# Kernel tuning notes

Hardware: AMD Instinct MI355X
Metric: run time of the kernel (lower is better)

## Reference

```python
import jax, jax.numpy as jnp
import numpy as np

RADIUS = 0.3      # extents/2, extents = radius_scale*6*particle_radius = 4*6*0.025 = 0.6
KSIZE = 4         # kernel_size [4,4,4]
KMAX = 80         # padded neighbor count
N = 50000
BOX = 5.2         # box side -> ~40 neighbors within RADIUS on average
CIN = 3
COUT = 3
_PI = 3.14159265358979323846


def _build_neighbors(pos, radius, kmax):
    # fixed-radius search (L2), ignore_query_point=True, padded to kmax per row
    n = pos.shape[0]
    r2 = radius * radius
    sq = (pos * pos).sum(1)
    idx = np.zeros((n, kmax), np.int32)
    msk = np.zeros((n, kmax), np.bool_)
    ch = 2500
    for s in range(0, n, ch):
        e = min(s + ch, n)
        d2 = sq[s:e, None] + sq[None, :] - 2.0 * (pos[s:e] @ pos.T)
        d2[np.arange(e - s), np.arange(s, e)] = np.inf  # radius_search_ignore_query_points
        rows, cols = np.nonzero(d2 < r2)
        starts = np.searchsorted(rows, np.arange(e - s))
        slot = np.arange(len(rows)) - starts[rows]
        keep = slot < kmax
        idx[rows[keep] + s, slot[keep]] = cols[keep]
        msk[rows[keep] + s, slot[keep]] = True
    return idx, msk


def setup_inputs():
    key = jax.random.key(0)
    k1, k2, k3 = jax.random.split(key, 3)
    pos = jax.random.uniform(k1, (N, 3), jnp.float32) * BOX
    vel = jax.random.normal(k2, (N, 3), jnp.float32)
    # keras 'uniform' initializer: U(-0.05, 0.05)
    kernel = jax.random.uniform(k3, (KSIZE, KSIZE, KSIZE, CIN, COUT), jnp.float32, -0.05, 0.05)
    nidx, nmask = _build_neighbors(np.asarray(pos), RADIUS, KMAX)
    return {"pos": pos, "vel": vel, "kernel": kernel,
            "neighbor_idx": jnp.asarray(nidx), "neighbor_mask": jnp.asarray(nmask)}


def _ball_to_cube_volume_preserving(u):
    # Open3D CoordinateTransformation.h: MapSphereToCylinder then MapCylinderToCube
    eps = 1e-12
    x, y, z = u[..., 0], u[..., 1], u[..., 2]
    sq = x * x + y * y + z * z
    norm = jnp.sqrt(jnp.maximum(sq, eps))
    sq_xy = x * x + y * y
    # sphere -> cylinder
    top = (1.25 * z * z) > sq_xy
    s_top = jnp.sqrt(3.0 * norm / (norm + jnp.abs(z)))
    s_side = norm / jnp.sqrt(jnp.maximum(sq_xy, eps))
    x1 = jnp.where(top, x * s_top, x * s_side)
    y1 = jnp.where(top, y * s_top, y * s_side)
    z1 = jnp.where(top, jnp.sign(z) * norm, 1.5 * z)
    small = sq < eps
    x1 = jnp.where(small, x, x1)
    y1 = jnp.where(small, y, y1)
    z1 = jnp.where(small, z, z1)
    # cylinder -> cube (equal-area disc->square on xy)
    sq_xy1 = x1 * x1 + y1 * y1
    norm_xy = jnp.sqrt(jnp.maximum(sq_xy1, eps))
    xbig = jnp.abs(y1) <= jnp.abs(x1)
    sx = jnp.sign(x1) * norm_xy
    sy = jnp.sign(y1) * norm_xy
    safe_x = jnp.where(jnp.abs(x1) > eps, x1, 1.0)
    safe_y = jnp.where(jnp.abs(y1) > eps, y1, 1.0)
    x2 = jnp.where(xbig, sx, sy * (4.0 / _PI) * jnp.arctan(x1 / safe_y))
    y2 = jnp.where(xbig, sx * (4.0 / _PI) * jnp.arctan(y1 / safe_x), sy)
    small_xy = sq_xy1 < eps
    x2 = jnp.where(small_xy, x1, x2)
    y2 = jnp.where(small_xy, y1, y2)
    return x2, y2, z1


def _grid_coords(c):
    # align_corners=True: [-1,1] -> [0, KSIZE-1]; 'linear' interpolation clamps to border
    t = jnp.clip((c + 1.0) * (0.5 * (KSIZE - 1)), 0.0, KSIZE - 1.0)
    t0 = jnp.floor(t)
    i0 = t0.astype(jnp.int32)
    i1 = jnp.minimum(i0 + 1, KSIZE - 1)
    f = t - t0
    return (i0, i1), (1.0 - f, f)


def _cconv(pos, vel, kernel, neighbor_idx, neighbor_mask):
    n = pos.shape[0]
    rel = pos[neighbor_idx] - pos[:, None, :]              # [N,K,3]
    d2 = jnp.sum(rel * rel, -1)
    # window_poly6 on squared distance normalized by radius^2
    imp = jnp.clip((1.0 - d2 / (RADIUS * RADIUS)) ** 3, 0.0, 1.0)
    imp = imp * neighbor_mask.astype(vel.dtype)
    cx, cy, cz = _ball_to_cube_volume_preserving(rel / RADIUS)
    (xi0, xi1), (wx0, wx1) = _grid_coords(cx)
    (yi0, yi1), (wy0, wy1) = _grid_coords(cy)
    (zi0, zi1), (wz0, wz1) = _grid_coords(cz)
    phi = vel[neighbor_idx] * imp[..., None]               # [N,K,Cin]
    rows = jnp.arange(n)[:, None]
    # accumulate window*trilinear-weighted features into the 64 filter taps,
    # then contract once with the flattened kernel (math identical to per-pair
    # interp(W) @ feat since everything is linear)
    A = jnp.zeros((n, KSIZE * KSIZE * KSIZE, vel.shape[1]), vel.dtype)
    for zi, wz in ((zi0, wz0), (zi1, wz1)):
        for yi, wy in ((yi0, wy0), (yi1, wy1)):
            for xi, wx in ((xi0, wx0), (xi1, wx1)):
                corner = (zi * KSIZE + yi) * KSIZE + xi
                A = A.at[rows, corner].add((wz * wy * wx)[..., None] * phi)
    Wflat = kernel.reshape(KSIZE * KSIZE * KSIZE, kernel.shape[3], kernel.shape[4])
    return jnp.einsum('ngi,gio->no', A, Wflat)        # [N, COUT]


def reference(pos, vel, kernel, neighbor_idx, neighbor_mask):
    return _cconv(pos, vel, kernel, neighbor_idx, neighbor_mask)
```

## Files before the change

### kernel.cpp

```cpp
#include <hip/hip_runtime.h>
#include <math.h>

#define N_PART 50000
#define KMAX 80
#define KS 4
#define LPP 16
#define MAXTRIP 5

typedef __attribute__((ext_vector_type(8))) _Float16 h8;
typedef __attribute__((ext_vector_type(2))) _Float16 h2;

__global__ __launch_bounds__(256) void pack_pv_kernel(
    const float* __restrict__ pos, const float* __restrict__ vel,
    float4* __restrict__ pv4)
{
    int p = blockIdx.x * blockDim.x + threadIdx.x;
    if (p >= N_PART) return;
    float4 a = make_float4(pos[3*p], pos[3*p+1], pos[3*p+2], vel[3*p]);
    float4 b = make_float4(vel[3*p+1], vel[3*p+2], 0.0f, 0.0f);
    pv4[2*p]     = a;
    pv4[2*p + 1] = b;
}

template <typename MT>
__device__ __forceinline__ int prefix_count(const MT* __restrict__ nmask, int base, int sub) {
    int lc = 0; bool more = true;
    #pragma unroll
    for (int i = 0; i < 5; ++i) {
        bool t = nmask[base + sub * 5 + i] != 0;
        lc += (more && t) ? 1 : 0;
        more = more && t;
    }
    bool full = (lc == 5);
    unsigned long long nb = __ballot(!full);
    int wl  = threadIdx.x & 63;
    int grp = wl >> 4;
    unsigned int gb = (unsigned int)((nb >> (16 * grp)) & 0xFFFFull);
    if (gb == 0) return KMAX;
    int fi  = __ffs(gb) - 1;
    int flc = __shfl(lc, (grp << 4) + fi, 64);
    return fi * 5 + flc;
}

__device__ __forceinline__ float atan_poly(float t) {
    float t2 = t * t;
    float p = -0.01172120f;
    p = p * t2 + 0.05265332f;
    p = p * t2 - 0.11643287f;
    p = p * t2 + 0.19354346f;
    p = p * t2 - 0.33262347f;
    p = p * t2 + 0.99997726f;
    return t * p;
}

template <bool PACKED>
__global__ __launch_bounds__(256) void cconv_kernel(
    const float* __restrict__ pos,
    const float* __restrict__ vel,
    const float4* __restrict__ pv4,
    const float* __restrict__ Wg,
    const int* __restrict__ nidx,
    const void* __restrict__ nmask,
    float* __restrict__ out)
{
    __shared__ _Float16 WsH[64 * 8];
    __shared__ float    Ws8[64];
    for (int t = threadIdx.x; t < 64 * 8; t += blockDim.x) {
        int g = t >> 3, r = t & 7;
        WsH[t] = (_Float16)Wg[g * 9 + r];
    }
    for (int t = threadIdx.x; t < 64; t += blockDim.x)
        Ws8[t] = Wg[t * 9 + 8];
    __syncthreads();

    int gid = blockIdx.x * blockDim.x + threadIdx.x;
    int p   = gid / LPP;
    int sub = gid & (LPP - 1);
    if (p >= N_PART) return;

    const int base = p * KMAX;

    int idxs[MAXTRIP];
    #pragma unroll
    for (int j = 0; j < MAXTRIP; ++j)
        idxs[j] = nidx[base + sub + j * LPP];

    bool byteMask;
    {
        const unsigned* mw = (const unsigned*)nmask;
        int lane = threadIdx.x & 63;
        bool big = false;
        #pragma unroll
        for (int i = 0; i < 8; ++i)
            big |= (mw[lane + 64 * i] > 1u);
        byteMask = (__ballot(big) != 0ULL);
    }

    float4 a, b;
    float  cpx, cpy, cpz;
    if (PACKED) {
        a = pv4[2 * idxs[0]];
        b = pv4[2 * idxs[0] + 1];
        float4 c = pv4[2 * p];
        cpx = c.x; cpy = c.y; cpz = c.z;
    } else {
        int i0 = idxs[0];
        a = make_float4(pos[i0*3], pos[i0*3+1], pos[i0*3+2], vel[i0*3]);
        b = make_float4(vel[i0*3+1], vel[i0*3+2], 0.f, 0.f);
        cpx = pos[p * 3 + 0]; cpy = pos[p * 3 + 1]; cpz = pos[p * 3 + 2];
    }

    int cnt;
    if (byteMask) cnt = prefix_count<unsigned char>((const unsigned char*)nmask, base, sub);
    else          cnt = prefix_count<int>((const int*)nmask, base, sub);

    int trips = (cnt > sub) ? ((cnt - sub + LPP - 1) >> 4) : 0;

    const float inv_r = 1.0f / 0.3f;
    const float eps   = 1e-12f;
    const float FOUR_OVER_PI = 1.27323954473516268615f;

    float acc0 = 0.0f, acc1 = 0.0f, acc2 = 0.0f;

    for (int j = 0; j < trips; ++j) {
        int jn = (j + 1 < MAXTRIP) ? j + 1 : MAXTRIP - 1;
        float4 an, bn;
        if (PACKED) {
            an = pv4[2 * idxs[jn]];
            bn = pv4[2 * idxs[jn] + 1];
        } else {
            int ii = idxs[jn];
            an = make_float4(pos[ii*3], pos[ii*3+1], pos[ii*3+2], vel[ii*3]);
            bn = make_float4(vel[ii*3+1], vel[ii*3+2], 0.f, 0.f);
        }

        float rx = (a.x - cpx) * inv_r;
        float ry = (a.y - cpy) * inv_r;
        float rz = (a.z - cpz) * inv_r;
        float ux = a.w, uy = b.x, uz = b.y;

        float sq = rx * rx + ry * ry + rz * rz;

        float t1  = 1.0f - sq;
        float imp = fminf(fmaxf(t1 * t1 * t1, 0.0f), 1.0f);

        float norm  = sqrtf(fmaxf(sq, eps));
        float sq_xy = rx * rx + ry * ry;
        bool  top   = (1.25f * rz * rz) > sq_xy;
        float s_top  = sqrtf(3.0f * norm * __builtin_amdgcn_rcpf(norm + fabsf(rz)));
        float s_side = norm * __builtin_amdgcn_rsqf(fmaxf(sq_xy, eps));
        float s  = top ? s_top : s_side;
        float x1 = rx * s;
        float y1 = ry * s;
        float z1 = top ? copysignf(norm, rz) : 1.5f * rz;
        if (sq < eps) { x1 = rx; y1 = ry; z1 = rz; }

        float sq_xy1  = x1 * x1 + y1 * y1;
        float norm_xy = sqrtf(fmaxf(sq_xy1, eps));
        bool  xbig = fabsf(y1) <= fabsf(x1);
        float num  = xbig ? y1 : x1;
        float den  = xbig ? x1 : y1;
        float sden = (fabsf(den) > eps) ? den : 1.0f;
        float t    = num * __builtin_amdgcn_rcpf(sden);
        float at   = atan_poly(t);
        float sd   = copysignf(norm_xy, den);
        float u    = sd * FOUR_OVER_PI * at;
        float x2   = xbig ? sd : u;
        float y2   = xbig ? u  : sd;
        if (sq_xy1 < eps) { x2 = x1; y2 = y1; }

        float tx = fminf(fmaxf((x2 + 1.0f) * 1.5f, 0.0f), 3.0f);
        float ty = fminf(fmaxf((y2 + 1.0f) * 1.5f, 0.0f), 3.0f);
        float tz = fminf(fmaxf((z1 + 1.0f) * 1.5f, 0.0f), 3.0f);
        float fx0 = floorf(tx), fy0 = floorf(ty), fz0 = floorf(tz);
        int xi0 = (int)fx0, yi0 = (int)fy0, zi0 = (int)fz0;
        int xi1 = min(xi0 + 1, KS - 1);
        int yi1 = min(yi0 + 1, KS - 1);
        int zi1 = min(zi0 + 1, KS - 1);
        float wx1 = tx - fx0, wx0 = 1.0f - wx1;
        float wy1 = ty - fy0, wy0 = 1.0f - wy1;
        float wz1 = tz - fz0, wz0 = 1.0f - wz1;

        int   zi[2] = { zi0, zi1 };  float wzv[2] = { wz0, wz1 };
        int   yi[2] = { yi0, yi1 };  float wyv[2] = { wy0, wy1 };
        int   xi[2] = { xi0, xi1 };  float wxv[2] = { wx0, wx1 };

        h2 M01 = (h2)(_Float16)0.0f;
        h2 M23 = (h2)(_Float16)0.0f;
        h2 M45 = (h2)(_Float16)0.0f;
        h2 M67 = (h2)(_Float16)0.0f;
        float m8 = 0.0f;

        #pragma unroll
        for (int cz = 0; cz < 2; ++cz) {
            #pragma unroll
            for (int cy = 0; cy < 2; ++cy) {
                float wzy = wzv[cz] * wyv[cy];
                #pragma unroll
                for (int cx = 0; cx < 2; ++cx) {
                    int corner = (zi[cz] * KS + yi[cy]) * KS + xi[cx];
                    h8 wv = *(const h8*)&WsH[corner << 3];
                    float wf = wzy * wxv[cx];
                    _Float16 wh = (_Float16)wf;
                    h2 ww = { wh, wh };
                    M01 += ww * __builtin_shufflevector(wv, wv, 0, 1);
                    M23 += ww * __builtin_shufflevector(wv, wv, 2, 3);
                    M45 += ww * __builtin_shufflevector(wv, wv, 4, 5);
                    M67 += ww * __builtin_shufflevector(wv, wv, 6, 7);
                    m8  += wf * Ws8[corner];
                }
            }
        }

        float m0 = (float)M01[0], m1 = (float)M01[1];
        float m2 = (float)M23[0], m3 = (float)M23[1];
        float m4 = (float)M45[0], m5 = (float)M45[1];
        float m6 = (float)M67[0], m7 = (float)M67[1];
        float s0 = ux * m0 + uy * m3 + uz * m6;
        float s1 = ux * m1 + uy * m4 + uz * m7;
        float s2 = ux * m2 + uy * m5 + uz * m8;
        acc0 += imp * s0;
        acc1 += imp * s1;
        acc2 += imp * s2;

        a = an; b = bn;
    }

    acc0 += __shfl_xor(acc0, 1); acc0 += __shfl_xor(acc0, 2);
    acc0 += __shfl_xor(acc0, 4); acc0 += __shfl_xor(acc0, 8);
    acc1 += __shfl_xor(acc1, 1); acc1 += __shfl_xor(acc1, 2);
    acc1 += __shfl_xor(acc1, 4); acc1 += __shfl_xor(acc1, 8);
    acc2 += __shfl_xor(acc2, 1); acc2 += __shfl_xor(acc2, 2);
    acc2 += __shfl_xor(acc2, 4); acc2 += __shfl_xor(acc2, 8);

    if (sub == 0) {
        out[p * 3 + 0] = acc0;
        out[p * 3 + 1] = acc1;
        out[p * 3 + 2] = acc2;
    }
}

extern "C" void kernel_launch(void* const* d_in, const int* in_sizes, int n_in,
                              void* d_out, int out_size, void* d_ws, size_t ws_size,
                              hipStream_t stream) {
    const float* pos   = (const float*)d_in[0];
    const float* vel   = (const float*)d_in[1];
    const float* Wg    = (const float*)d_in[2];
    const int*   nidx  = (const int*)d_in[3];
    const void*  nmask = d_in[4];
    float*       out   = (float*)d_out;

    size_t pv_off = 256;
    size_t need   = pv_off + (size_t)N_PART * 8 * sizeof(float);
    bool   packed = ws_size >= need;
    float4* pv4   = (float4*)((char*)d_ws + pv_off);

    if (packed) {
        pack_pv_kernel<<<(N_PART + 255) / 256, 256, 0, stream>>>(pos, vel, pv4);
    }

    int threads = 256;
    long long total = (long long)N_PART * LPP;
    int grid = (int)((total + threads - 1) / threads);
    if (packed) {
        cconv_kernel<true><<<grid, threads, 0, stream>>>(pos, vel, pv4, Wg, nidx, nmask, out);
    } else {
        cconv_kernel<false><<<grid, threads, 0, stream>>>(pos, vel, (const float4*)nullptr, Wg, nidx, nmask, out);
    }
}
```

Measured before the change: 33.77 us.

## Drop pack kernel and process two neighbors per iteration with deeper prefetch

Removes the separate pos/vel packing kernel and its launch, reading the pos and vel arrays directly with scalar loads instead. The neighbor loop is unrolled by two and prefetches two neighbors' data ahead, masking the second pair's contribution when it falls past the valid count. This aims to cut a kernel launch and an extra global pass, and to raise memory-level parallelism per thread. The costs are unaligned scalar gathers replacing float4 loads, more registers, and wasted work on masked pairs.

```diff
diff --git a/kernel.cpp b/kernel.cpp
--- a/kernel.cpp
+++ b/kernel.cpp
@@ -5,21 +5,19 @@
 #define KMAX 80
 #define KS 4
 #define LPP 16
-#define MAXTRIP 5
 
 typedef __attribute__((ext_vector_type(8))) _Float16 h8;
 typedef __attribute__((ext_vector_type(2))) _Float16 h2;
 
-__global__ __launch_bounds__(256) void pack_pv_kernel(
-    const float* __restrict__ pos, const float* __restrict__ vel,
-    float4* __restrict__ pv4)
-{
-    int p = blockIdx.x * blockDim.x + threadIdx.x;
-    if (p >= N_PART) return;
-    float4 a = make_float4(pos[3*p], pos[3*p+1], pos[3*p+2], vel[3*p]);
-    float4 b = make_float4(vel[3*p+1], vel[3*p+2], 0.0f, 0.0f);
-    pv4[2*p]     = a;
-    pv4[2*p + 1] = b;
+__device__ __forceinline__ float atan_poly(float t) {
+    float t2 = t * t;
+    float p = -0.01172120f;
+    p = p * t2 + 0.05265332f;
+    p = p * t2 - 0.11643287f;
+    p = p * t2 + 0.19354346f;
+    p = p * t2 - 0.33262347f;
+    p = p * t2 + 0.99997726f;
+    return t * p;
 }
 
 template <typename MT>
@@ -42,22 +40,116 @@
     return fi * 5 + flc;
 }
 
-__device__ __forceinline__ float atan_poly(float t) {
-    float t2 = t * t;
-    float p = -0.01172120f;
-    p = p * t2 + 0.05265332f;
-    p = p * t2 - 0.11643287f;
-    p = p * t2 + 0.19354346f;
-    p = p * t2 - 0.33262347f;
-    p = p * t2 + 0.99997726f;
-    return t * p;
-}
-
-template <bool PACKED>
+struct PV { float px, py, pz, ux, uy, uz; };
+
+__device__ __forceinline__ void load_pv(const float* __restrict__ pos,
+                                        const float* __restrict__ vel,
+                                        int i, PV& v) {
+    v.px = pos[3*i];  v.py = pos[3*i+1];  v.pz = pos[3*i+2];
+    v.ux = vel[3*i];  v.uy = vel[3*i+1];  v.uz = vel[3*i+2];
+}
+
+__device__ __forceinline__ void pair_contrib(
+    const PV& n, float cpx, float cpy, float cpz, float vmask,
+    const _Float16* __restrict__ WsH, const float* __restrict__ Ws8,
+    float& acc0, float& acc1, float& acc2)
+{
+    const float inv_r = 1.0f / 0.3f;
+    const float eps   = 1e-12f;
+    const float FOUR_OVER_PI = 1.27323954473516268615f;
+
+    float rx = (n.px - cpx) * inv_r;
+    float ry = (n.py - cpy) * inv_r;
+    float rz = (n.pz - cpz) * inv_r;
+
+    float sq = rx * rx + ry * ry + rz * rz;
+
+    float t1  = 1.0f - sq;
+    float imp = fminf(fmaxf(t1 * t1 * t1, 0.0f), 1.0f) * vmask;
+
+    float norm  = sqrtf(fmaxf(sq, eps));
+    float sq_xy = rx * rx + ry * ry;
+    bool  top   = (1.25f * rz * rz) > sq_xy;
+    float s_top  = sqrtf(3.0f * norm * __builtin_amdgcn_rcpf(norm + fabsf(rz)));
+    float s_side = norm * __builtin_amdgcn_rsqf(fmaxf(sq_xy, eps));
+    float s  = top ? s_top : s_side;
+    float x1 = rx * s;
+    float y1 = ry * s;
+    float z1 = top ? copysignf(norm, rz) : 1.5f * rz;
+    if (sq < eps) { x1 = rx; y1 = ry; z1 = rz; }
+
+    float sq1 = x1 * x1 + y1 * y1;
+    float nxy = sqrtf(fmaxf(sq1, eps));
+    bool  xb  = fabsf(y1) <= fabsf(x1);
+    float num = xb ? y1 : x1;
+    float den = xb ? x1 : y1;
+    float sden = (fabsf(den) > eps) ? den : 1.0f;
+    float t    = num * __builtin_amdgcn_rcpf(sden);
+    float at   = atan_poly(t);
+    float sd   = copysignf(nxy, den);
+    float u    = sd * FOUR_OVER_PI * at;
+    float x2   = xb ? sd : u;
+    float y2   = xb ? u  : sd;
+    if (sq1 < eps) { x2 = x1; y2 = y1; }
+
+    float tx = fminf(fmaxf((x2 + 1.0f) * 1.5f, 0.0f), 3.0f);
+    float ty = fminf(fmaxf((y2 + 1.0f) * 1.5f, 0.0f), 3.0f);
+    float tz = fminf(fmaxf((z1 + 1.0f) * 1.5f, 0.0f), 3.0f);
+    float fx0 = floorf(tx), fy0 = floorf(ty), fz0 = floorf(tz);
+    int xi0 = (int)fx0, yi0 = (int)fy0, zi0 = (int)fz0;
+    int xi1 = min(xi0 + 1, KS - 1);
+    int yi1 = min(yi0 + 1, KS - 1);
+    int zi1 = min(zi0 + 1, KS - 1);
+    float wx1 = tx - fx0, wx0 = 1.0f - wx1;
+    float wy1 = ty - fy0, wy0 = 1.0f - wy1;
+    float wz1 = tz - fz0, wz0 = 1.0f - wz1;
+
+    int   zia[2] = { zi0, zi1 };  float wza[2] = { wz0, wz1 };
+    int   yia[2] = { yi0, yi1 };  float wya[2] = { wy0, wy1 };
+    int   xia[2] = { xi0, xi1 };  float wxa[2] = { wx0, wx1 };
+
+    h2 M01 = (h2)(_Float16)0.0f;
+    h2 M23 = (h2)(_Float16)0.0f;
+    h2 M45 = (h2)(_Float16)0.0f;
+    h2 M67 = (h2)(_Float16)0.0f;
+    float m8 = 0.0f;
+
+    #pragma unroll
+    for (int cz = 0; cz < 2; ++cz) {
+        #pragma unroll
+        for (int cy = 0; cy < 2; ++cy) {
+            float wzy = wza[cz] * wya[cy];
+            #pragma unroll
+            for (int cx = 0; cx < 2; ++cx) {
+                int corner = (zia[cz] * KS + yia[cy]) * KS + xia[cx];
+                h8 wv = *(const h8*)&WsH[corner << 3];
+                float wf = wzy * wxa[cx];
+                _Float16 wh = (_Float16)wf;
+                h2 ww = { wh, wh };
+                M01 += ww * __builtin_shufflevector(wv, wv, 0, 1);
+                M23 += ww * __builtin_shufflevector(wv, wv, 2, 3);
+                M45 += ww * __builtin_shufflevector(wv, wv, 4, 5);
+                M67 += ww * __builtin_shufflevector(wv, wv, 6, 7);
+                m8  += wf * Ws8[corner];
+            }
+        }
+    }
+
+    float m0 = (float)M01[0], m1 = (float)M01[1];
+    float m2 = (float)M23[0], m3 = (float)M23[1];
+    float m4 = (float)M45[0], m5 = (float)M45[1];
+    float m6 = (float)M67[0], m7 = (float)M67[1];
+    float s0 = n.ux * m0 + n.uy * m3 + n.uz * m6;
+    float s1 = n.ux * m1 + n.uy * m4 + n.uz * m7;
+    float s2 = n.ux * m2 + n.uy * m5 + n.uz * m8;
+    acc0 += imp * s0;
+    acc1 += imp * s1;
+    acc2 += imp * s2;
+}
+
 __global__ __launch_bounds__(256) void cconv_kernel(
     const float* __restrict__ pos,
     const float* __restrict__ vel,
-    const float4* __restrict__ pv4,
     const float* __restrict__ Wg,
     const int* __restrict__ nidx,
     const void* __restrict__ nmask,
@@ -74,16 +166,16 @@
     __syncthreads();
 
     int gid = blockIdx.x * blockDim.x + threadIdx.x;
-    int p   = gid / LPP;
-    int sub = gid & (LPP - 1);
+    int p   = gid >> 4;
+    int sub = gid & 15;
     if (p >= N_PART) return;
 
     const int base = p * KMAX;
 
-    int idxs[MAXTRIP];
+    int idxs[5];
     #pragma unroll
-    for (int j = 0; j < MAXTRIP; ++j)
-        idxs[j] = nidx[base + sub + j * LPP];
+    for (int m = 0; m < 5; ++m)
+        idxs[m] = nidx[base + sub + (m << 4)];
 
     bool byteMask;
     {
@@ -96,134 +188,34 @@
         byteMask = (__ballot(big) != 0ULL);
     }
 
-    float4 a, b;
-    float  cpx, cpy, cpz;
-    if (PACKED) {
-        a = pv4[2 * idxs[0]];
-        b = pv4[2 * idxs[0] + 1];
-        float4 c = pv4[2 * p];
-        cpx = c.x; cpy = c.y; cpz = c.z;
-    } else {
-        int i0 = idxs[0];
-        a = make_float4(pos[i0*3], pos[i0*3+1], pos[i0*3+2], vel[i0*3]);
-        b = make_float4(vel[i0*3+1], vel[i0*3+2], 0.f, 0.f);
-        cpx = pos[p * 3 + 0]; cpy = pos[p * 3 + 1]; cpz = pos[p * 3 + 2];
-    }
+    float cpx = pos[3 * p], cpy = pos[3 * p + 1], cpz = pos[3 * p + 2];
 
     int cnt;
     if (byteMask) cnt = prefix_count<unsigned char>((const unsigned char*)nmask, base, sub);
     else          cnt = prefix_count<int>((const int*)nmask, base, sub);
 
-    int trips = (cnt > sub) ? ((cnt - sub + LPP - 1) >> 4) : 0;
-
-    const float inv_r = 1.0f / 0.3f;
-    const float eps   = 1e-12f;
-    const float FOUR_OVER_PI = 1.27323954473516268615f;
+    int rem   = cnt - sub;
+    int trips = (rem > 0) ? ((rem + 31) >> 5) : 0;
+
+    PV A0, A1, A0n, A1n;
+    load_pv(pos, vel, idxs[0], A0);
+    load_pv(pos, vel, idxs[1], A1);
 
     float acc0 = 0.0f, acc1 = 0.0f, acc2 = 0.0f;
 
     for (int j = 0; j < trips; ++j) {
-        int jn = (j + 1 < MAXTRIP) ? j + 1 : MAXTRIP - 1;
-        float4 an, bn;
-        if (PACKED) {
-            an = pv4[2 * idxs[jn]];
-            bn = pv4[2 * idxs[jn] + 1];
-        } else {
-            int ii = idxs[jn];
-            an = make_float4(pos[ii*3], pos[ii*3+1], pos[ii*3+2], vel[ii*3]);
-            bn = make_float4(vel[ii*3+1], vel[ii*3+2], 0.f, 0.f);
-        }
-
-        float rx = (a.x - cpx) * inv_r;
-        float ry = (a.y - cpy) * inv_r;
-        float rz = (a.z - cpz) * inv_r;
-        float ux = a.w, uy = b.x, uz = b.y;
-
-        float sq = rx * rx + ry * ry + rz * rz;
-
-        float t1  = 1.0f - sq;
-        float imp = fminf(fmaxf(t1 * t1 * t1, 0.0f), 1.0f);
-
-        float norm  = sqrtf(fmaxf(sq, eps));
-        float sq_xy = rx * rx + ry * ry;
-        bool  top   = (1.25f * rz * rz) > sq_xy;
-        float s_top  = sqrtf(3.0f * norm * __builtin_amdgcn_rcpf(norm + fabsf(rz)));
-        float s_side = norm * __builtin_amdgcn_rsqf(fmaxf(sq_xy, eps));
-        float s  = top ? s_top : s_side;
-        float x1 = rx * s;
-        float y1 = ry * s;
-        float z1 = top ? copysignf(norm, rz) : 1.5f * rz;
-        if (sq < eps) { x1 = rx; y1 = ry; z1 = rz; }
-
-        float sq_xy1  = x1 * x1 + y1 * y1;
-        float norm_xy = sqrtf(fmaxf(sq_xy1, eps));
-        bool  xbig = fabsf(y1) <= fabsf(x1);
-        float num  = xbig ? y1 : x1;
-        float den  = xbig ? x1 : y1;
-        float sden = (fabsf(den) > eps) ? den : 1.0f;
-        float t    = num * __builtin_amdgcn_rcpf(sden);
-        float at   = atan_poly(t);
-        float sd   = copysignf(norm_xy, den);
-        float u    = sd * FOUR_OVER_PI * at;
-        float x2   = xbig ? sd : u;
-        float y2   = xbig ? u  : sd;
-        if (sq_xy1 < eps) { x2 = x1; y2 = y1; }
-
-        float tx = fminf(fmaxf((x2 + 1.0f) * 1.5f, 0.0f), 3.0f);
-        float ty = fminf(fmaxf((y2 + 1.0f) * 1.5f, 0.0f), 3.0f);
-        float tz = fminf(fmaxf((z1 + 1.0f) * 1.5f, 0.0f), 3.0f);
-        float fx0 = floorf(tx), fy0 = floorf(ty), fz0 = floorf(tz);
-        int xi0 = (int)fx0, yi0 = (int)fy0, zi0 = (int)fz0;
-        int xi1 = min(xi0 + 1, KS - 1);
-        int yi1 = min(yi0 + 1, KS - 1);
-        int zi1 = min(zi0 + 1, KS - 1);
-        float wx1 = tx - fx0, wx0 = 1.0f - wx1;
-        float wy1 = ty - fy0, wy0 = 1.0f - wy1;
-        float wz1 = tz - fz0, wz0 = 1.0f - wz1;
-
-        int   zi[2] = { zi0, zi1 };  float wzv[2] = { wz0, wz1 };
-        int   yi[2] = { yi0, yi1 };  float wyv[2] = { wy0, wy1 };
-        int   xi[2] = { xi0, xi1 };  float wxv[2] = { wx0, wx1 };
-
-        h2 M01 = (h2)(_Float16)0.0f;
-        h2 M23 = (h2)(_Float16)0.0f;
-        h2 M45 = (h2)(_Float16)0.0f;
-        h2 M67 = (h2)(_Float16)0.0f;
-        float m8 = 0.0f;
-
-        #pragma unroll
-        for (int cz = 0; cz < 2; ++cz) {
-            #pragma unroll
-            for (int cy = 0; cy < 2; ++cy) {
-                float wzy = wzv[cz] * wyv[cy];
-                #pragma unroll
-                for (int cx = 0; cx < 2; ++cx) {
-                    int corner = (zi[cz] * KS + yi[cy]) * KS + xi[cx];
-                    h8 wv = *(const h8*)&WsH[corner << 3];
-                    float wf = wzy * wxv[cx];
-                    _Float16 wh = (_Float16)wf;
-                    h2 ww = { wh, wh };
-                    M01 += ww * __builtin_shufflevector(wv, wv, 0, 1);
-                    M23 += ww * __builtin_shufflevector(wv, wv, 2, 3);
-                    M45 += ww * __builtin_shufflevector(wv, wv, 4, 5);
-                    M67 += ww * __builtin_shufflevector(wv, wv, 6, 7);
-                    m8  += wf * Ws8[corner];
-                }
-            }
-        }
-
-        float m0 = (float)M01[0], m1 = (float)M01[1];
-        float m2 = (float)M23[0], m3 = (float)M23[1];
-        float m4 = (float)M45[0], m5 = (float)M45[1];
-        float m6 = (float)M67[0], m7 = (float)M67[1];
-        float s0 = ux * m0 + uy * m3 + uz * m6;
-        float s1 = ux * m1 + uy * m4 + uz * m7;
-        float s2 = ux * m2 + uy * m5 + uz * m8;
-        acc0 += imp * s0;
-        acc1 += imp * s1;
-        acc2 += imp * s2;
-
-        a = an; b = bn;
+        int mn0 = min(2 * j + 2, 4);
+        int mn1 = min(2 * j + 3, 4);
+        load_pv(pos, vel, idxs[mn0], A0n);
+        load_pv(pos, vel, idxs[mn1], A1n);
+
+        int   k1 = sub + ((2 * j + 1) << 4);
+        float v1 = (k1 < cnt) ? 1.0f : 0.0f;
+
+        pair_contrib(A0, cpx, cpy, cpz, 1.0f, WsH, Ws8, acc0, acc1, acc2);
+        pair_contrib(A1, cpx, cpy, cpz, v1,   WsH, Ws8, acc0, acc1, acc2);
+
+        A0 = A0n; A1 = A1n;
     }
 
     acc0 += __shfl_xor(acc0, 1); acc0 += __shfl_xor(acc0, 2);
@@ -250,21 +242,8 @@
     const void*  nmask = d_in[4];
     float*       out   = (float*)d_out;
 
-    size_t pv_off = 256;
-    size_t need   = pv_off + (size_t)N_PART * 8 * sizeof(float);
-    bool   packed = ws_size >= need;
-    float4* pv4   = (float4*)((char*)d_ws + pv_off);
-
-    if (packed) {
-        pack_pv_kernel<<<(N_PART + 255) / 256, 256, 0, stream>>>(pos, vel, pv4);
-    }
-
     int threads = 256;
     long long total = (long long)N_PART * LPP;
     int grid = (int)((total + threads - 1) / threads);
-    if (packed) {
-        cconv_kernel<true><<<grid, threads, 0, stream>>>(pos, vel, pv4, Wg, nidx, nmask, out);
-    } else {
-        cconv_kernel<false><<<grid, threads, 0, stream>>>(pos, vel, (const float4*)nullptr, Wg, nidx, nmask, out);
-    }
-}
+    cconv_kernel<<<grid, threads, 0, stream>>>(pos, vel, Wg, nidx, nmask, out);
+}
```

Result: faster. 33.05 us (-2.1%).
